# Kernel tuning notes

Hardware: AMD Instinct MI355X
Metric: run time of the kernel (lower is better)

## Reference

```python
import jax, jax.numpy as jnp
import numpy as np

NUM_HEADS = 16
ROPE_THETA = 10000.0
SEQ = 2048
D_MODEL = 2048


def _rope(x):
    # x: (seq, heads, head_dim). Equinox RotaryPositionalEmbedding:
    # rotate_half variant with tiled (non-interleaved) cos/sin.
    S, H, hd = x.shape
    half = hd // 2
    freqs = 1.0 / (ROPE_THETA ** (jnp.arange(0, half, dtype=jnp.float32) * 2.0 / hd))  # (half,)
    t = jnp.arange(S, dtype=jnp.float32)
    angles = jnp.outer(t, freqs)  # (S, half)
    cos = jnp.tile(jnp.cos(angles), (1, 2))[:, None, :]  # (S, 1, hd)
    sin = jnp.tile(jnp.sin(angles), (1, 2))[:, None, :]
    x1, x2 = jnp.split(x, 2, axis=-1)
    rot = jnp.concatenate((-x2, x1), axis=-1)  # rotate_half
    return (x * cos + rot * sin).astype(x.dtype)


def setup_inputs() -> dict:
    key = jax.random.key(0)
    ks = jax.random.split(key, 7)
    mk = lambda k, scale=1.0: (jax.random.normal(k, (SEQ, D_MODEL), dtype=jnp.float32) * scale)
    return {
        "query": mk(ks[0]),
        "key_": mk(ks[1]),
        "value": mk(ks[2]),
        "Wq": jax.random.normal(ks[3], (D_MODEL, D_MODEL), dtype=jnp.float32) / np.sqrt(D_MODEL),
        "Wk": jax.random.normal(ks[4], (D_MODEL, D_MODEL), dtype=jnp.float32) / np.sqrt(D_MODEL),
        "Wv": jax.random.normal(ks[5], (D_MODEL, D_MODEL), dtype=jnp.float32) / np.sqrt(D_MODEL),
        "Wo": jax.random.normal(ks[6], (D_MODEL, D_MODEL), dtype=jnp.float32) / np.sqrt(D_MODEL),
    }


def reference(query, key_, value, Wq, Wk, Wv, Wo):
    S, D = query.shape
    H = NUM_HEADS
    hd = D // H
    # QKV projections (equinox Linear: y = W @ x, vmapped over seq -> x @ W.T)
    q = (query @ Wq.T).reshape(S, H, hd)
    k = (key_ @ Wk.T).reshape(S, H, hd)
    v = (value @ Wv.T).reshape(S, H, hd)
    # Per-head RoPE on q and k
    q = _rope(q)
    k = _rope(k)
    # Causal attention, scale 1/sqrt(head_dim) (dropout_p=0, inference)
    attn = jax.nn.dot_product_attention(q[None], k[None], v[None], is_causal=True)[0]  # (S, H, hd)
    # Output projection
    return attn.reshape(S, D) @ Wo.T
```

## Files before the change

kernel.cpp:

```cpp
#include <hip/hip_runtime.h>

typedef unsigned short u16;
typedef __attribute__((ext_vector_type(8))) __bf16 bf16x8;
typedef __attribute__((ext_vector_type(4))) float f32x4;

#define D_MODEL 2048
#define SEQ 2048
#define NHEAD 16
#define HDIM 128

#define AS1 __attribute__((address_space(1)))
#define AS3 __attribute__((address_space(3)))
#define GL2LDS(g, l) __builtin_amdgcn_global_load_lds((AS1 const void*)(g), (AS3 void*)(l), 16, 0, 0)

__device__ __forceinline__ u16 f2bf(float f) {
  unsigned u = __float_as_uint(f);
  u += 0x7fff + ((u >> 16) & 1);
  return (u16)(u >> 16);
}
__device__ __forceinline__ float bf2f(u16 h) {
  return __uint_as_float(((unsigned)h) << 16);
}
__device__ __forceinline__ float fexp2(float x) {
#if __has_builtin(__builtin_amdgcn_exp2f)
  return __builtin_amdgcn_exp2f(x);
#else
  return __expf(x * 0.69314718055994531f);
#endif
}

__global__ __launch_bounds__(256) void k_cast7(const float* i0, const float* i1, const float* i2,
                                               const float* i3, const float* i4, const float* i5,
                                               const float* i6,
                                               u16* o0, u16* o1, u16* o2, u16* o3, u16* o4,
                                               u16* o5, u16* o6) {
  const float* in; u16* out;
  switch (blockIdx.y) {
    case 0: in = i0; out = o0; break;
    case 1: in = i1; out = o1; break;
    case 2: in = i2; out = o2; break;
    case 3: in = i3; out = o3; break;
    case 4: in = i4; out = o4; break;
    case 5: in = i5; out = o5; break;
    default: in = i6; out = o6; break;
  }
  const int i = blockIdx.x * blockDim.x + threadIdx.x;
  const float4 v = reinterpret_cast<const float4*>(in)[i];
  ushort4 o;
  o.x = f2bf(v.x); o.y = f2bf(v.y); o.z = f2bf(v.z); o.w = f2bf(v.w);
  reinterpret_cast<ushort4*>(out)[i] = o;
}

__device__ __forceinline__ void stage128(const u16* __restrict__ P, u16* dst, int row0, int kt,
                                         int t, int w) {
#pragma unroll
  for (int c = 0; c < 4; ++c) {
    const int r = (c * 2048 + t * 8) >> 6;
    const int ch = ((t & 7) ^ (r & 7)) * 8;
    GL2LDS(P + (size_t)(row0 + r) * D_MODEL + kt + ch, dst + c * 2048 + w * 512);
  }
}
__device__ __forceinline__ void stage64(const u16* __restrict__ P, u16* dst, int row0, int kt,
                                        int t, int w) {
#pragma unroll
  for (int c = 0; c < 2; ++c) {
    const int r = (c * 2048 + t * 8) >> 6;
    const int ch = ((t & 7) ^ (r & 7)) * 8;
    GL2LDS(P + (size_t)(row0 + r) * D_MODEL + kt + ch, dst + c * 2048 + w * 512);
  }
}

__device__ __forceinline__ void gemm_nt_body(const u16* __restrict__ A, const u16* __restrict__ B,
                                             void* __restrict__ C, u16* As0, u16* As1,
                                             u16* Bs0, u16* Bs1, int outmode) {
  const int tn = blockIdx.x, tm = blockIdx.y;
  const int t = threadIdx.x;
  const int lane = t & 63, w = t >> 6;
  const int wr = w >> 1, wc = w & 1;
  const int lrow = lane & 15, g = lane >> 4;
  f32x4 acc[4][4] = {};

  stage128(A, As0, tm * 128, 0, t, w);
  stage128(B, Bs0, tn * 128, 0, t, w);
  __syncthreads();

  u16 *Ar = As0, *Br = Bs0, *Aw = As1, *Bw = Bs1;
#pragma unroll 1
  for (int kt = 0; kt < D_MODEL; kt += 64) {
    if (kt + 64 < D_MODEL) {
      stage128(A, Aw, tm * 128, kt + 64, t, w);
      stage128(B, Bw, tn * 128, kt + 64, t, w);
    }
#pragma unroll
    for (int kk = 0; kk < 2; ++kk) {
      bf16x8 af[4], bfr[4];
#pragma unroll
      for (int i = 0; i < 4; ++i) {
        const int sw = (((kk << 2) + g) ^ (lrow & 7)) * 8;
        af[i]  = *(const bf16x8*)(Ar + (wr * 64 + i * 16 + lrow) * 64 + sw);
        bfr[i] = *(const bf16x8*)(Br + (wc * 64 + i * 16 + lrow) * 64 + sw);
      }
#pragma unroll
      for (int i = 0; i < 4; ++i)
#pragma unroll
        for (int j = 0; j < 4; ++j)
          acc[i][j] = __builtin_amdgcn_mfma_f32_16x16x32_bf16(af[i], bfr[j], acc[i][j], 0, 0, 0);
    }
    __syncthreads();
    u16* tp;
    tp = Ar; Ar = Aw; Aw = tp;
    tp = Br; Br = Bw; Bw = tp;
  }

  const int crow0 = tm * 128 + wr * 64 + (lane >> 4) * 4;
  const int ccol0 = tn * 128 + wc * 64 + lrow;
  if (outmode == 2) {
#pragma unroll
    for (int i = 0; i < 4; ++i)
#pragma unroll
      for (int j = 0; j < 4; ++j) {
        ushort4 o;
        o.x = f2bf(acc[i][j][0]); o.y = f2bf(acc[i][j][1]);
        o.z = f2bf(acc[i][j][2]); o.w = f2bf(acc[i][j][3]);
        *(ushort4*)((u16*)C + (size_t)(ccol0 + j * 16) * D_MODEL + crow0 + i * 16) = o;
      }
  } else {
#pragma unroll
    for (int i = 0; i < 4; ++i)
#pragma unroll
      for (int j = 0; j < 4; ++j)
#pragma unroll
        for (int r = 0; r < 4; ++r)
          ((u16*)C)[(size_t)(crow0 + i * 16 + r) * D_MODEL + ccol0 + j * 16] = f2bf(acc[i][j][r]);
  }
}

__global__ __launch_bounds__(256, 2) void k_gemm_qkv(const u16* Xq, const u16* Xk, const u16* Xv,
                                                     const u16* Wq, const u16* Wk, const u16* Wv,
                                                     u16* Q, u16* K, u16* VT) {
  __shared__ u16 As[2][128 * 64], Bs[2][128 * 64];
  const int z = blockIdx.z;
  const u16* A = (z == 0) ? Xq : (z == 1) ? Xk : Xv;
  const u16* B = (z == 0) ? Wq : (z == 1) ? Wk : Wv;
  u16* C = (z == 0) ? Q : (z == 1) ? K : VT;
  gemm_nt_body(A, B, C, As[0], As[1], Bs[0], Bs[1], (z == 2) ? 2 : 0);
}

__global__ __launch_bounds__(256, 2) void k_gemm_out(const u16* __restrict__ A, const u16* __restrict__ B,
                                                     float* __restrict__ C) {
  __shared__ u16 As[2][128 * 64], Bs[2][64 * 64];
  const int tn = blockIdx.x, tm = blockIdx.y;
  const int t = threadIdx.x;
  const int lane = t & 63, w = t >> 6;
  const int wr = w >> 1, wc = w & 1;
  const int lrow = lane & 15, g = lane >> 4;
  f32x4 acc[4][2] = {};

  stage128(A, As[0], tm * 128, 0, t, w);
  stage64(B, Bs[0], tn * 64, 0, t, w);
  __syncthreads();

  u16 *Ar = As[0], *Br = Bs[0], *Aw = As[1], *Bw = Bs[1];
#pragma unroll 1
  for (int kt = 0; kt < D_MODEL; kt += 64) {
    if (kt + 64 < D_MODEL) {
      stage128(A, Aw, tm * 128, kt + 64, t, w);
      stage64(B, Bw, tn * 64, kt + 64, t, w);
    }
#pragma unroll
    for (int kk = 0; kk < 2; ++kk) {
      bf16x8 af[4], bfr[2];
#pragma unroll
      for (int i = 0; i < 4; ++i) {
        const int sw = (((kk << 2) + g) ^ (lrow & 7)) * 8;
        af[i] = *(const bf16x8*)(Ar + (wr * 64 + i * 16 + lrow) * 64 + sw);
        if (i < 2) bfr[i] = *(const bf16x8*)(Br + (wc * 32 + i * 16 + lrow) * 64 + sw);
      }
#pragma unroll
      for (int i = 0; i < 4; ++i)
#pragma unroll
        for (int j = 0; j < 2; ++j)
          acc[i][j] = __builtin_amdgcn_mfma_f32_16x16x32_bf16(af[i], bfr[j], acc[i][j], 0, 0, 0);
    }
    __syncthreads();
    u16* tp;
    tp = Ar; Ar = Aw; Aw = tp;
    tp = Br; Br = Bw; Bw = tp;
  }
  const int crow0 = tm * 128 + wr * 64 + (lane >> 4) * 4;
  const int ccol0 = tn * 64 + wc * 32 + lrow;
#pragma unroll
  for (int i = 0; i < 4; ++i)
#pragma unroll
    for (int j = 0; j < 2; ++j)
#pragma unroll
      for (int r = 0; r < 4; ++r)
        C[(size_t)(crow0 + i * 16 + r) * D_MODEL + ccol0 + j * 16] = acc[i][j][r];
}

__global__ __launch_bounds__(256) void k_rope(u16* Q, u16* K) {
  const int idx = blockIdx.x * blockDim.x + threadIdx.x;
  u16* X = blockIdx.y ? K : Q;
  const float scale = blockIdx.y ? 1.0f : (1.4426950408889634f * 0.08838834764831845f);
  const int s = idx >> 10;
  const int h = (idx >> 6) & 15;
  const int j = idx & 63;
  const float freq = __expf((float)j * -0.14391156831212787f);
  float sn, cs;
  sincosf((float)s * freq, &sn, &cs);
  const size_t base = (size_t)s * D_MODEL + h * HDIM + j;
  const float x1 = bf2f(X[base]), x2 = bf2f(X[base + 64]);
  X[base]      = f2bf((x1 * cs - x2 * sn) * scale);
  X[base + 64] = f2bf((x2 * cs + x1 * sn) * scale);
}

__global__ __launch_bounds__(256, 2) void k_attn(const u16* __restrict__ Q, const u16* __restrict__ K,
                                                 const u16* __restrict__ VT, u16* __restrict__ O) {
  __shared__ u16 Kb[2][64 * 128];
  __shared__ u16 Vb[2][128 * 64];
  __shared__ u16 Pl[4][32 * 64];
  const int bx = blockIdx.x;
  const int h = bx & 15;
  const int qt = 31 - (bx >> 4);
  const int t = threadIdx.x;
  const int lane = t & 63, w = t >> 6;
  const int mh = w & 1, par = w >> 1;
  const int lrow = lane & 15, g = lane >> 4, lk = g * 8;
  const int qrow0 = qt * 64 + mh * 32;

  bf16x8 qf[2][4];
#pragma unroll
  for (int mi = 0; mi < 2; ++mi)
#pragma unroll
    for (int ks = 0; ks < 4; ++ks)
      qf[mi][ks] = *(const bf16x8*)(Q + (size_t)(qrow0 + mi * 16 + lrow) * D_MODEL + h * HDIM + ks * 32 + lk);

  f32x4 accO[2][8] = {};
  float m_run[2][4], l_run[2][4];
#pragma unroll
  for (int mi = 0; mi < 2; ++mi)
#pragma unroll
    for (int r = 0; r < 4; ++r) { m_run[mi][r] = -1e30f; l_run[mi][r] = 0.f; }

  const int nt = qt + 1;
  const int nss = (nt + 1) >> 1;
#pragma unroll 1
  for (int s = 0; s < nss; ++s) {
    const int t0 = 2 * s;
    const int t1 = (2 * s + 1 < nt) ? 2 * s + 1 : nt - 1;
#pragma unroll
    for (int i = 0; i < 4; ++i) {
      const int rk = w * 16 + i * 4 + (lane >> 4);
      const int ck = lane & 15;
      GL2LDS(K + (size_t)(t0 * 64 + rk) * D_MODEL + h * HDIM + ((ck ^ (rk & 15)) * 8),
             Kb[0] + (w * 16 + i * 4) * 128);
      GL2LDS(K + (size_t)(t1 * 64 + rk) * D_MODEL + h * HDIM + ((ck ^ (rk & 15)) * 8),
             Kb[1] + (w * 16 + i * 4) * 128);
      const int rv = w * 32 + i * 8 + (lane >> 3);
      const int cv = lane & 7;
      GL2LDS(VT + (size_t)(h * HDIM + rv) * D_MODEL + t0 * 64 + ((cv ^ (rv & 7)) * 8),
             Vb[0] + (w * 32 + i * 8) * 64);
      GL2LDS(VT + (size_t)(h * HDIM + rv) * D_MODEL + t1 * 64 + ((cv ^ (rv & 7)) * 8),
             Vb[1] + (w * 32 + i * 8) * 64);
    }
    __syncthreads();

    const int T = 2 * s + par;
    if (T < nt) {
      f32x4 sc[2][4] = {};
#pragma unroll
      for (int ks = 0; ks < 4; ++ks) {
        bf16x8 kf[4];
#pragma unroll
        for (int ni = 0; ni < 4; ++ni)
          kf[ni] = *(const bf16x8*)(&Kb[par][(ni * 16 + lrow) * 128 + ((ks * 4 + g) ^ lrow) * 8]);
#pragma unroll
        for (int mi = 0; mi < 2; ++mi)
#pragma unroll
          for (int ni = 0; ni < 4; ++ni)
            sc[mi][ni] = __builtin_amdgcn_mfma_f32_16x16x32_bf16(qf[mi][ks], kf[ni], sc[mi][ni], 0, 0, 0);
      }

      if (T == qt) {
        const int kv = T * 64;
#pragma unroll
        for (int mi = 0; mi < 2; ++mi)
#pragma unroll
          for (int ni = 0; ni < 4; ++ni) {
            const int colg = kv + ni * 16 + lrow;
#pragma unroll
            for (int r = 0; r < 4; ++r) {
              const int rowg = qrow0 + mi * 16 + g * 4 + r;
              if (colg > rowg) sc[mi][ni][r] = -1e30f;
            }
          }
      }

#pragma unroll
      for (int mi = 0; mi < 2; ++mi)
#pragma unroll
        for (int r = 0; r < 4; ++r) {
          float pm = fmaxf(fmaxf(sc[mi][0][r], sc[mi][1][r]), fmaxf(sc[mi][2][r], sc[mi][3][r]));
          pm = fmaxf(pm, __shfl_xor(pm, 1));
          pm = fmaxf(pm, __shfl_xor(pm, 2));
          pm = fmaxf(pm, __shfl_xor(pm, 4));
          pm = fmaxf(pm, __shfl_xor(pm, 8));
          const float mo = m_run[mi][r];
          const float mn = fmaxf(mo, pm);
          const float sf = fexp2(mo - mn);
          float rs = 0.f;
#pragma unroll
          for (int ni = 0; ni < 4; ++ni) {
            const float p = fexp2(sc[mi][ni][r] - mn);
            sc[mi][ni][r] = p;
            rs += p;
          }
          rs += __shfl_xor(rs, 1);
          rs += __shfl_xor(rs, 2);
          rs += __shfl_xor(rs, 4);
          rs += __shfl_xor(rs, 8);
          l_run[mi][r] = l_run[mi][r] * sf + rs;
          m_run[mi][r] = mn;
#pragma unroll
          for (int dt = 0; dt < 8; ++dt) accO[mi][dt][r] *= sf;
        }

#pragma unroll
      for (int mi = 0; mi < 2; ++mi)
#pragma unroll
        for (int ni = 0; ni < 4; ++ni)
#pragma unroll
          for (int r = 0; r < 4; ++r) {
            const int row = mi * 16 + g * 4 + r;
            const int chnk = (2 * ni + (lrow >> 3)) ^ (row & 7);
            Pl[w][row * 64 + chnk * 8 + (lrow & 7)] = f2bf(sc[mi][ni][r]);
          }
      asm volatile("s_waitcnt lgkmcnt(0)" ::: "memory");

#pragma unroll
      for (int ks2 = 0; ks2 < 2; ++ks2) {
        bf16x8 pf[2];
#pragma unroll
        for (int mi = 0; mi < 2; ++mi) {
          const int row = mi * 16 + lrow;
          pf[mi] = *(const bf16x8*)(&Pl[w][row * 64 + ((ks2 * 4 + g) ^ (row & 7)) * 8]);
        }
#pragma unroll
        for (int dt = 0; dt < 8; ++dt) {
          const int R = dt * 16 + lrow;
          const bf16x8 vf = *(const bf16x8*)(&Vb[par][R * 64 + ((ks2 * 4 + g) ^ (R & 7)) * 8]);
#pragma unroll
          for (int mi = 0; mi < 2; ++mi)
            accO[mi][dt] = __builtin_amdgcn_mfma_f32_16x16x32_bf16(pf[mi], vf, accO[mi][dt], 0, 0, 0);
        }
      }
    }
    __syncthreads();
  }

  float* mrg = (float*)&Kb[0][0];
  float* mlb = (float*)&Vb[0][0];
  if (par == 1) {
#pragma unroll
    for (int mi = 0; mi < 2; ++mi)
#pragma unroll
      for (int dt = 0; dt < 8; ++dt)
#pragma unroll
        for (int r = 0; r < 4; ++r)
          mrg[mh * 4096 + (mi * 16 + g * 4 + r) * 128 + dt * 16 + lrow] = accO[mi][dt][r];
#pragma unroll
    for (int mi = 0; mi < 2; ++mi)
#pragma unroll
      for (int r = 0; r < 4; ++r) {
        const int row = mi * 16 + g * 4 + r;
        mlb[mh * 64 + row * 2]     = m_run[mi][r];
        mlb[mh * 64 + row * 2 + 1] = l_run[mi][r];
      }
  }
  __syncthreads();
  if (par == 0) {
#pragma unroll
    for (int mi = 0; mi < 2; ++mi)
#pragma unroll
      for (int r = 0; r < 4; ++r) {
        const int row = mi * 16 + g * 4 + r;
        const float m1 = mlb[mh * 64 + row * 2];
        const float l1 = mlb[mh * 64 + row * 2 + 1];
        const float mn = fmaxf(m_run[mi][r], m1);
        const float f0 = fexp2(m_run[mi][r] - mn);
        const float f1 = fexp2(m1 - mn);
        const float inv = 1.0f / (l_run[mi][r] * f0 + l1 * f1);
        const size_t grow = (size_t)(qrow0 + row);
#pragma unroll
        for (int dt = 0; dt < 8; ++dt) {
          const float v1 = mrg[mh * 4096 + row * 128 + dt * 16 + lrow];
          O[grow * D_MODEL + h * HDIM + dt * 16 + lrow] =
              f2bf((accO[mi][dt][r] * f0 + v1 * f1) * inv);
        }
      }
  }
}

extern "C" void kernel_launch(void* const* d_in, const int* in_sizes, int n_in,
                              void* d_out, int out_size, void* d_ws, size_t ws_size,
                              hipStream_t stream) {
  const float* query = (const float*)d_in[0];
  const float* key_  = (const float*)d_in[1];
  const float* value = (const float*)d_in[2];
  const float* Wq    = (const float*)d_in[3];
  const float* Wk    = (const float*)d_in[4];
  const float* Wv    = (const float*)d_in[5];
  const float* Wo    = (const float*)d_in[6];
  float* out = (float*)d_out;

  const size_t TS = (size_t)SEQ * D_MODEL;
  u16* ws  = (u16*)d_ws;
  u16* bXq = ws + 0 * TS;
  u16* bXk = ws + 1 * TS;
  u16* bXv = ws + 2 * TS;
  u16* bWq = ws + 3 * TS;
  u16* bWk = ws + 4 * TS;
  u16* bWv = ws + 5 * TS;
  u16* bWo = ws + 6 * TS;
  u16* bQ  = ws + 7 * TS;
  u16* bK  = ws + 8 * TS;
  u16* bVT = ws + 9 * TS;
  u16* bA  = ws + 10 * TS;

  const int n4 = (int)(TS / 4);
  k_cast7<<<dim3(n4 / 256, 7), 256, 0, stream>>>(query, key_, value, Wq, Wk, Wv, Wo,
                                                 bXq, bXk, bXv, bWq, bWk, bWv, bWo);

  k_gemm_qkv<<<dim3(16, 16, 3), 256, 0, stream>>>(bXq, bXk, bXv, bWq, bWk, bWv, bQ, bK, bVT);

  k_rope<<<dim3((SEQ * NHEAD * 64) / 256, 2), 256, 0, stream>>>(bQ, bK);

  k_attn<<<dim3(512), 256, 0, stream>>>(bQ, bK, bVT, bA);

  k_gemm_out<<<dim3(32, 16), 256, 0, stream>>>(bA, bWo, out);
}
```

Before: 310.2 us.

## Use split-K 128x128 output GEMM, lazy softmax rescale, smaller P tile

```diff
diff --git a/kernel.cpp b/kernel.cpp
--- a/kernel.cpp
+++ b/kernel.cpp
@@ -51,19 +51,14 @@
   reinterpret_cast<ushort4*>(out)[i] = o;
 }
 
+__global__ __launch_bounds__(256) void k_zero(float4* C) {
+  C[blockIdx.x * blockDim.x + threadIdx.x] = float4{0.f, 0.f, 0.f, 0.f};
+}
+
 __device__ __forceinline__ void stage128(const u16* __restrict__ P, u16* dst, int row0, int kt,
                                          int t, int w) {
 #pragma unroll
   for (int c = 0; c < 4; ++c) {
-    const int r = (c * 2048 + t * 8) >> 6;
-    const int ch = ((t & 7) ^ (r & 7)) * 8;
-    GL2LDS(P + (size_t)(row0 + r) * D_MODEL + kt + ch, dst + c * 2048 + w * 512);
-  }
-}
-__device__ __forceinline__ void stage64(const u16* __restrict__ P, u16* dst, int row0, int kt,
-                                        int t, int w) {
-#pragma unroll
-  for (int c = 0; c < 2; ++c) {
     const int r = (c * 2048 + t * 8) >> 6;
     const int ch = ((t & 7) ^ (r & 7)) * 8;
     GL2LDS(P + (size_t)(row0 + r) * D_MODEL + kt + ch, dst + c * 2048 + w * 512);
@@ -148,38 +143,39 @@
 
 __global__ __launch_bounds__(256, 2) void k_gemm_out(const u16* __restrict__ A, const u16* __restrict__ B,
                                                      float* __restrict__ C) {
-  __shared__ u16 As[2][128 * 64], Bs[2][64 * 64];
+  __shared__ u16 As[2][128 * 64], Bs[2][128 * 64];
   const int tn = blockIdx.x, tm = blockIdx.y;
+  const int kbase = blockIdx.z * 1024;
   const int t = threadIdx.x;
   const int lane = t & 63, w = t >> 6;
   const int wr = w >> 1, wc = w & 1;
   const int lrow = lane & 15, g = lane >> 4;
-  f32x4 acc[4][2] = {};
-
-  stage128(A, As[0], tm * 128, 0, t, w);
-  stage64(B, Bs[0], tn * 64, 0, t, w);
+  f32x4 acc[4][4] = {};
+
+  stage128(A, As[0], tm * 128, kbase, t, w);
+  stage128(B, Bs[0], tn * 128, kbase, t, w);
   __syncthreads();
 
   u16 *Ar = As[0], *Br = Bs[0], *Aw = As[1], *Bw = Bs[1];
 #pragma unroll 1
-  for (int kt = 0; kt < D_MODEL; kt += 64) {
-    if (kt + 64 < D_MODEL) {
-      stage128(A, Aw, tm * 128, kt + 64, t, w);
-      stage64(B, Bw, tn * 64, kt + 64, t, w);
+  for (int kt = 0; kt < 1024; kt += 64) {
+    if (kt + 64 < 1024) {
+      stage128(A, Aw, tm * 128, kbase + kt + 64, t, w);
+      stage128(B, Bw, tn * 128, kbase + kt + 64, t, w);
     }
 #pragma unroll
     for (int kk = 0; kk < 2; ++kk) {
-      bf16x8 af[4], bfr[2];
+      bf16x8 af[4], bfr[4];
 #pragma unroll
       for (int i = 0; i < 4; ++i) {
         const int sw = (((kk << 2) + g) ^ (lrow & 7)) * 8;
-        af[i] = *(const bf16x8*)(Ar + (wr * 64 + i * 16 + lrow) * 64 + sw);
-        if (i < 2) bfr[i] = *(const bf16x8*)(Br + (wc * 32 + i * 16 + lrow) * 64 + sw);
+        af[i]  = *(const bf16x8*)(Ar + (wr * 64 + i * 16 + lrow) * 64 + sw);
+        bfr[i] = *(const bf16x8*)(Br + (wc * 64 + i * 16 + lrow) * 64 + sw);
       }
 #pragma unroll
       for (int i = 0; i < 4; ++i)
 #pragma unroll
-        for (int j = 0; j < 2; ++j)
+        for (int j = 0; j < 4; ++j)
           acc[i][j] = __builtin_amdgcn_mfma_f32_16x16x32_bf16(af[i], bfr[j], acc[i][j], 0, 0, 0);
     }
     __syncthreads();
@@ -188,14 +184,14 @@
     tp = Br; Br = Bw; Bw = tp;
   }
   const int crow0 = tm * 128 + wr * 64 + (lane >> 4) * 4;
-  const int ccol0 = tn * 64 + wc * 32 + lrow;
+  const int ccol0 = tn * 128 + wc * 64 + lrow;
 #pragma unroll
   for (int i = 0; i < 4; ++i)
 #pragma unroll
-    for (int j = 0; j < 2; ++j)
+    for (int j = 0; j < 4; ++j)
 #pragma unroll
       for (int r = 0; r < 4; ++r)
-        C[(size_t)(crow0 + i * 16 + r) * D_MODEL + ccol0 + j * 16] = acc[i][j][r];
+        atomicAdd(&C[(size_t)(crow0 + i * 16 + r) * D_MODEL + ccol0 + j * 16], acc[i][j][r]);
 }
 
 __global__ __launch_bounds__(256) void k_rope(u16* Q, u16* K) {
@@ -218,7 +214,7 @@
                                                  const u16* __restrict__ VT, u16* __restrict__ O) {
   __shared__ u16 Kb[2][64 * 128];
   __shared__ u16 Vb[2][128 * 64];
-  __shared__ u16 Pl[4][32 * 64];
+  __shared__ u16 Pl[4][32 * 32];
   const int bx = blockIdx.x;
   const int h = bx & 15;
   const int qt = 31 - (bx >> 4);
@@ -306,12 +302,17 @@
           pm = fmaxf(pm, __shfl_xor(pm, 4));
           pm = fmaxf(pm, __shfl_xor(pm, 8));
           const float mo = m_run[mi][r];
-          const float mn = fmaxf(mo, pm);
-          const float sf = fexp2(mo - mn);
+          const bool defer = __all(pm - mo <= 8.f);
+          float base = mo, sf = 1.0f;
+          if (!defer) {
+            base = fmaxf(mo, pm);
+            sf = fexp2(mo - base);
+            m_run[mi][r] = base;
+          }
           float rs = 0.f;
 #pragma unroll
           for (int ni = 0; ni < 4; ++ni) {
-            const float p = fexp2(sc[mi][ni][r] - mn);
+            const float p = fexp2(sc[mi][ni][r] - base);
             sc[mi][ni][r] = p;
             rs += p;
           }
@@ -319,31 +320,35 @@
           rs += __shfl_xor(rs, 2);
           rs += __shfl_xor(rs, 4);
           rs += __shfl_xor(rs, 8);
-          l_run[mi][r] = l_run[mi][r] * sf + rs;
-          m_run[mi][r] = mn;
-#pragma unroll
-          for (int dt = 0; dt < 8; ++dt) accO[mi][dt][r] *= sf;
+          l_run[mi][r] = fmaf(l_run[mi][r], sf, rs);
+          if (!defer) {
+#pragma unroll
+            for (int dt = 0; dt < 8; ++dt) accO[mi][dt][r] *= sf;
+          }
         }
 
 #pragma unroll
-      for (int mi = 0; mi < 2; ++mi)
-#pragma unroll
-        for (int ni = 0; ni < 4; ++ni)
-#pragma unroll
-          for (int r = 0; r < 4; ++r) {
-            const int row = mi * 16 + g * 4 + r;
-            const int chnk = (2 * ni + (lrow >> 3)) ^ (row & 7);
-            Pl[w][row * 64 + chnk * 8 + (lrow & 7)] = f2bf(sc[mi][ni][r]);
+      for (int ks2 = 0; ks2 < 2; ++ks2) {
+#pragma unroll
+        for (int mi = 0; mi < 2; ++mi)
+#pragma unroll
+          for (int nh = 0; nh < 2; ++nh) {
+            const int ni = ks2 * 2 + nh;
+#pragma unroll
+            for (int r = 0; r < 4; ++r) {
+              const int row = mi * 16 + g * 4 + r;
+              const int sw = (row + (row >> 2)) & 3;
+              const int ch = (nh * 2 + (lrow >> 3)) ^ sw;
+              Pl[w][row * 32 + ch * 8 + (lrow & 7)] = f2bf(sc[mi][ni][r]);
+            }
           }
-      asm volatile("s_waitcnt lgkmcnt(0)" ::: "memory");
-
-#pragma unroll
-      for (int ks2 = 0; ks2 < 2; ++ks2) {
+        asm volatile("s_waitcnt lgkmcnt(0)" ::: "memory");
         bf16x8 pf[2];
 #pragma unroll
         for (int mi = 0; mi < 2; ++mi) {
           const int row = mi * 16 + lrow;
-          pf[mi] = *(const bf16x8*)(&Pl[w][row * 64 + ((ks2 * 4 + g) ^ (row & 7)) * 8]);
+          const int sw = (row + (row >> 2)) & 3;
+          pf[mi] = *(const bf16x8*)(&Pl[w][row * 32 + (g ^ sw) * 8]);
         }
 #pragma unroll
         for (int dt = 0; dt < 8; ++dt) {
@@ -437,5 +442,6 @@
 
   k_attn<<<dim3(512), 256, 0, stream>>>(bQ, bK, bVT, bA);
 
-  k_gemm_out<<<dim3(32, 16), 256, 0, stream>>>(bA, bWo, out);
-}
+  k_zero<<<dim3(4096), 256, 0, stream>>>((float4*)out);
+  k_gemm_out<<<dim3(16, 16, 2), 256, 0, stream>>>(bA, bWo, out);
+}
```

After: 342.1 us. 1.1x slower.
